# Kernel optimization log

Measured on AMD Instinct MI355X. Metric: run time of the kernel, lower is better.

Reference implementation:

```python
import jax, jax.numpy as jnp
import numpy as np

B, S, C = 16, 2048, 256      # batch, seq_len, in_channels
QK, H = 256, 8               # qk_dim, num_heads
N, ED = 512, 256             # envbook_num+1, envbook_dim
D = QK // H                  # per_head_dim
SCALING = QK ** (-0.5)       # note: original scales by full qk_dim, not per-head dim


def setup_inputs() -> dict:
    key = jax.random.key(0)
    k1, k2, k3, k4 = jax.random.split(key, 4)
    x = jax.random.normal(k1, (B, S, C), dtype=jnp.float32)
    env_codebook = jax.random.normal(k2, (N, ED), dtype=jnp.float32)
    # nn.Linear weights stored transposed for x @ W convention
    Wq = jax.random.normal(k3, (C, QK), dtype=jnp.float32) * (1.0 / np.sqrt(C))
    Wk = jax.random.normal(k4, (ED, QK), dtype=jnp.float32) * (1.0 / np.sqrt(ED))
    return {"x": x, "env_codebook": env_codebook, "Wq": Wq, "Wk": Wk}


def reference(x, env_codebook, Wq, Wk):
    # query: [B,S,QK] -> [B,S,H,D]; key: [N,QK] -> [N,H,D]
    q = (x @ Wq).reshape(B, S, H, D)
    k = (env_codebook @ Wk).reshape(N, H, D)
    # scores: [B,H,S,N]
    scores = jnp.einsum("bshd,nhd->bhsn", q, k) * SCALING
    probs = jax.nn.softmax(scores, axis=-1)
    causal_att = probs[..., 0]          # [B,H,S]
    env_selects = probs[..., 1:]        # [B,H,S,N-1]
    env_att = env_selects.sum(axis=-1)  # [B,H,S]
    return (env_att, causal_att, env_selects)
```

## Files before the change

### kernel.cpp

```cpp
#include <hip/hip_runtime.h>
#include <hip/hip_bf16.h>

#define B_  16
#define S_  2048
#define C_  256
#define QK_ 256
#define H_  8
#define N_  512
#define D_  32

typedef short  bf16x8 __attribute__((ext_vector_type(8)));
typedef float  f32x4  __attribute__((ext_vector_type(4)));

__device__ __forceinline__ unsigned short f2bf(float f) {
    union { float f; unsigned u; } v; v.f = f;
    unsigned r = v.u + 0x7fffu + ((v.u >> 16) & 1u);
    return (unsigned short)(r >> 16);
}

__global__ void k_convert_x(const float* __restrict__ x,
                            unsigned short* __restrict__ xbf) {
    int i = blockIdx.x * blockDim.x + threadIdx.x;
    float4 v = ((const float4*)x)[i];
    ushort4 o;
    o.x = f2bf(v.x); o.y = f2bf(v.y); o.z = f2bf(v.z); o.w = f2bf(v.w);
    ((ushort4*)xbf)[i] = o;
}

__global__ void k_wqt(const float* __restrict__ Wq,
                      unsigned short* __restrict__ wqt) {
    int n = blockIdx.x, c = threadIdx.x;
    wqt[n * 256 + c] = f2bf(Wq[c * 256 + n]);
}

__global__ void k_kproj(const float* __restrict__ env,
                        const float* __restrict__ Wk,
                        unsigned short* __restrict__ kbf) {
    __shared__ float erow[256];
    int n = blockIdx.x, t = threadIdx.x;
    erow[t] = env[n * 256 + t];
    __syncthreads();
    float acc = 0.f;
#pragma unroll 8
    for (int c = 0; c < 256; ++c) acc += erow[c] * Wk[c * 256 + t];
    int h = t >> 5, d = t & 31;
    kbf[(h * N_ + n) * D_ + d] = f2bf(acc);
}

__global__ __launch_bounds__(256) void k_qproj(
        const unsigned short* __restrict__ xbf,
        const unsigned short* __restrict__ wqt,
        unsigned short* __restrict__ qws) {
    int tid  = threadIdx.x;
    int lane = tid & 63, w = tid >> 6;
    int l15  = lane & 15, quad = lane >> 4;
    int r0   = blockIdx.x * 16;
    int nb   = w * 64;

    const unsigned short* arow = xbf + (size_t)(r0 + l15) * 256 + quad * 8;
    const unsigned short* brow[4];
#pragma unroll
    for (int nt = 0; nt < 4; ++nt)
        brow[nt] = wqt + (size_t)(nb + nt * 16 + l15) * 256 + quad * 8;

    f32x4 acc[4] = {};
#pragma unroll
    for (int kk = 0; kk < 8; ++kk) {
        bf16x8 a = *(const bf16x8*)(arow + kk * 32);
#pragma unroll
        for (int nt = 0; nt < 4; ++nt) {
            bf16x8 b = *(const bf16x8*)(brow[nt] + kk * 32);
            acc[nt] = __builtin_amdgcn_mfma_f32_16x16x32_bf16(a, b, acc[nt], 0, 0, 0);
        }
    }
#pragma unroll
    for (int nt = 0; nt < 4; ++nt) {
        int col = nb + nt * 16 + l15;
        int h = col >> 5, d = col & 31;
#pragma unroll
        for (int r = 0; r < 4; ++r) {
            int gr = r0 + quad * 4 + r;
            int b = gr >> 11, s = gr & 2047;
            qws[(((size_t)(b * H_ + h)) * S_ + s) * D_ + d] = f2bf(acc[nt][r] * 0.0625f);
        }
    }
}

__global__ __launch_bounds__(256) void k_scores(
        const unsigned short* __restrict__ qws,
        const unsigned short* __restrict__ kbf,
        float* __restrict__ out) {
    float* env_att = out;
    float* causal  = out + (size_t)B_ * H_ * S_;
    float* es      = out + (size_t)2 * B_ * H_ * S_;

    int tid  = threadIdx.x;
    int lane = tid & 63, w = tid >> 6;
    int l15  = lane & 15, quad = lane >> 4;

    int bid  = blockIdx.x;
    int bh   = bid >> 4;
    int sblk = (bid & 15) * 128;
    int h    = bh & 7;

    __shared__ float red[4][16];

    const unsigned short* kb = kbf + (size_t)h * N_ * D_;
    int nb = w * 128;
    bf16x8 bf[8];
#pragma unroll
    for (int j = 0; j < 8; ++j)
        bf[j] = *(const bf16x8*)(kb + (size_t)(nb + j * 16 + l15) * D_ + quad * 8);

    const unsigned short* qbase = qws + (size_t)bh * S_ * D_;

    for (int st = 0; st < 8; ++st) {
        int s0 = sblk + st * 16;
        bf16x8 a = *(const bf16x8*)(qbase + (size_t)(s0 + l15) * D_ + quad * 8);

        f32x4 c[8];
#pragma unroll
        for (int j = 0; j < 8; ++j) {
            f32x4 z = {};
            c[j] = __builtin_amdgcn_mfma_f32_16x16x32_bf16(a, bf[j], z, 0, 0, 0);
        }
        float psum[4] = {0.f, 0.f, 0.f, 0.f};
#pragma unroll
        for (int j = 0; j < 8; ++j)
#pragma unroll
            for (int r = 0; r < 4; ++r) {
                float e = __expf(c[j][r]);
                c[j][r] = e;
                psum[r] += e;
            }
#pragma unroll
        for (int off = 1; off < 16; off <<= 1)
#pragma unroll
            for (int r = 0; r < 4; ++r)
                psum[r] += __shfl_xor(psum[r], off, 64);
        if (l15 == 0) {
#pragma unroll
            for (int r = 0; r < 4; ++r) red[w][quad * 4 + r] = psum[r];
        }
        __syncthreads();
        float inv[4];
#pragma unroll
        for (int r = 0; r < 4; ++r) {
            int row = quad * 4 + r;
            float tot = red[0][row] + red[1][row] + red[2][row] + red[3][row];
            inv[r] = 1.0f / tot;
        }
        __syncthreads();

        int srow = bh * S_ + s0 + quad * 4;
#pragma unroll
        for (int j = 0; j < 8; ++j) {
            int n = nb + j * 16 + l15;
#pragma unroll
            for (int r = 0; r < 4; ++r) {
                float p = c[j][r] * inv[r];
                if (n > 0) es[(size_t)(srow + r) * 511 + (n - 1)] = p;
            }
        }
        if (w == 0 && l15 == 0) {
#pragma unroll
            for (int r = 0; r < 4; ++r) {
                float p0 = c[0][r] * inv[r];
                causal[srow + r]  = p0;
                env_att[srow + r] = 1.0f - p0;
            }
        }
    }
}

extern "C" void kernel_launch(void* const* d_in, const int* in_sizes, int n_in,
                              void* d_out, int out_size, void* d_ws, size_t ws_size,
                              hipStream_t stream) {
    const float* x   = (const float*)d_in[0];
    const float* env = (const float*)d_in[1];
    const float* Wq  = (const float*)d_in[2];
    const float* Wk  = (const float*)d_in[3];
    float* out = (float*)d_out;

    char* ws = (char*)d_ws;
    unsigned short* xbf = (unsigned short*)(ws);
    unsigned short* qws = (unsigned short*)(ws + 16777216);
    unsigned short* kbf = (unsigned short*)(ws + 33554432);
    unsigned short* wqt = (unsigned short*)(ws + 33816576);

    k_convert_x<<<8192, 256, 0, stream>>>(x, xbf);
    k_wqt      <<<256,  256, 0, stream>>>(Wq, wqt);
    k_kproj    <<<512,  256, 0, stream>>>(env, Wk, kbf);
    k_qproj    <<<2048, 256, 0, stream>>>(xbf, wqt, qws);
    k_scores   <<<2048, 256, 0, stream>>>(qws, kbf, out);
}
```

Measured before the change: 669.9 us.

## Fuse x conversion into Q projection, merge prep kernels, stage score stores in LDS

```diff
diff --git a/kernel.cpp b/kernel.cpp
--- a/kernel.cpp
+++ b/kernel.cpp
@@ -18,37 +18,29 @@
     return (unsigned short)(r >> 16);
 }
 
-__global__ void k_convert_x(const float* __restrict__ x,
-                            unsigned short* __restrict__ xbf) {
-    int i = blockIdx.x * blockDim.x + threadIdx.x;
-    float4 v = ((const float4*)x)[i];
-    ushort4 o;
-    o.x = f2bf(v.x); o.y = f2bf(v.y); o.z = f2bf(v.z); o.w = f2bf(v.w);
-    ((ushort4*)xbf)[i] = o;
-}
-
-__global__ void k_wqt(const float* __restrict__ Wq,
-                      unsigned short* __restrict__ wqt) {
-    int n = blockIdx.x, c = threadIdx.x;
-    wqt[n * 256 + c] = f2bf(Wq[c * 256 + n]);
-}
-
-__global__ void k_kproj(const float* __restrict__ env,
-                        const float* __restrict__ Wk,
-                        unsigned short* __restrict__ kbf) {
+__global__ void k_prep(const float* __restrict__ Wq,
+                       const float* __restrict__ env,
+                       const float* __restrict__ Wk,
+                       unsigned short* __restrict__ wqt,
+                       unsigned short* __restrict__ kbf) {
     __shared__ float erow[256];
-    int n = blockIdx.x, t = threadIdx.x;
-    erow[t] = env[n * 256 + t];
-    __syncthreads();
-    float acc = 0.f;
+    int bid = blockIdx.x, t = threadIdx.x;
+    if (bid < 256) {
+        wqt[bid * 256 + t] = f2bf(Wq[t * 256 + bid]);
+    } else {
+        int n = bid - 256;
+        erow[t] = env[n * 256 + t];
+        __syncthreads();
+        float acc = 0.f;
 #pragma unroll 8
-    for (int c = 0; c < 256; ++c) acc += erow[c] * Wk[c * 256 + t];
-    int h = t >> 5, d = t & 31;
-    kbf[(h * N_ + n) * D_ + d] = f2bf(acc);
+        for (int c = 0; c < 256; ++c) acc += erow[c] * Wk[c * 256 + t];
+        int h = t >> 5, d = t & 31;
+        kbf[(h * N_ + n) * D_ + d] = f2bf(acc);
+    }
 }
 
 __global__ __launch_bounds__(256) void k_qproj(
-        const unsigned short* __restrict__ xbf,
+        const float* __restrict__ x,
         const unsigned short* __restrict__ wqt,
         unsigned short* __restrict__ qws) {
     int tid  = threadIdx.x;
@@ -57,7 +49,7 @@
     int r0   = blockIdx.x * 16;
     int nb   = w * 64;
 
-    const unsigned short* arow = xbf + (size_t)(r0 + l15) * 256 + quad * 8;
+    const float* arow = x + (size_t)(r0 + l15) * 256 + quad * 8;
     const unsigned short* brow[4];
 #pragma unroll
     for (int nt = 0; nt < 4; ++nt)
@@ -66,7 +58,13 @@
     f32x4 acc[4] = {};
 #pragma unroll
     for (int kk = 0; kk < 8; ++kk) {
-        bf16x8 a = *(const bf16x8*)(arow + kk * 32);
+        float4 f0 = *(const float4*)(arow + kk * 32);
+        float4 f1 = *(const float4*)(arow + kk * 32 + 4);
+        bf16x8 a;
+        a[0] = (short)f2bf(f0.x); a[1] = (short)f2bf(f0.y);
+        a[2] = (short)f2bf(f0.z); a[3] = (short)f2bf(f0.w);
+        a[4] = (short)f2bf(f1.x); a[5] = (short)f2bf(f1.y);
+        a[6] = (short)f2bf(f1.z); a[7] = (short)f2bf(f1.w);
 #pragma unroll
         for (int nt = 0; nt < 4; ++nt) {
             bf16x8 b = *(const bf16x8*)(brow[nt] + kk * 32);
@@ -86,6 +84,7 @@
     }
 }
 
+#define PADW 514
 __global__ __launch_bounds__(256) void k_scores(
         const unsigned short* __restrict__ qws,
         const unsigned short* __restrict__ kbf,
@@ -93,6 +92,9 @@
     float* env_att = out;
     float* causal  = out + (size_t)B_ * H_ * S_;
     float* es      = out + (size_t)2 * B_ * H_ * S_;
+
+    __shared__ float red[4][16];
+    __shared__ float tile[16 * PADW];
 
     int tid  = threadIdx.x;
     int lane = tid & 63, w = tid >> 6;
@@ -102,8 +104,6 @@
     int bh   = bid >> 4;
     int sblk = (bid & 15) * 128;
     int h    = bh & 7;
-
-    __shared__ float red[4][16];
 
     const unsigned short* kb = kbf + (size_t)h * N_ * D_;
     int nb = w * 128;
@@ -150,25 +150,29 @@
             float tot = red[0][row] + red[1][row] + red[2][row] + red[3][row];
             inv[r] = 1.0f / tot;
         }
-        __syncthreads();
-
-        int srow = bh * S_ + s0 + quad * 4;
 #pragma unroll
         for (int j = 0; j < 8; ++j) {
             int n = nb + j * 16 + l15;
 #pragma unroll
-            for (int r = 0; r < 4; ++r) {
-                float p = c[j][r] * inv[r];
-                if (n > 0) es[(size_t)(srow + r) * 511 + (n - 1)] = p;
-            }
+            for (int r = 0; r < 4; ++r)
+                tile[(quad * 4 + r) * PADW + n] = c[j][r] * inv[r];
         }
         if (w == 0 && l15 == 0) {
+            int srow = bh * S_ + s0 + quad * 4;
 #pragma unroll
             for (int r = 0; r < 4; ++r) {
                 float p0 = c[0][r] * inv[r];
                 causal[srow + r]  = p0;
                 env_att[srow + r] = 1.0f - p0;
             }
+        }
+        __syncthreads();
+        size_t region = ((size_t)bh * S_ + s0) * 511;
+#pragma unroll
+        for (int row = 0; row < 16; ++row) {
+            es[region + row * 511 + tid] = tile[row * PADW + 1 + tid];
+            if (tid < 255)
+                es[region + row * 511 + 256 + tid] = tile[row * PADW + 257 + tid];
         }
     }
 }
@@ -183,14 +187,11 @@
     float* out = (float*)d_out;
 
     char* ws = (char*)d_ws;
-    unsigned short* xbf = (unsigned short*)(ws);
-    unsigned short* qws = (unsigned short*)(ws + 16777216);
-    unsigned short* kbf = (unsigned short*)(ws + 33554432);
-    unsigned short* wqt = (unsigned short*)(ws + 33816576);
+    unsigned short* qws = (unsigned short*)(ws);
+    unsigned short* kbf = (unsigned short*)(ws + 16777216);
+    unsigned short* wqt = (unsigned short*)(ws + 17039360);
 
-    k_convert_x<<<8192, 256, 0, stream>>>(x, xbf);
-    k_wqt      <<<256,  256, 0, stream>>>(Wq, wqt);
-    k_kproj    <<<512,  256, 0, stream>>>(env, Wk, kbf);
-    k_qproj    <<<2048, 256, 0, stream>>>(xbf, wqt, qws);
-    k_scores   <<<2048, 256, 0, stream>>>(qws, kbf, out);
+    k_prep  <<<768,  256, 0, stream>>>(Wq, env, Wk, wqt, kbf);
+    k_qproj <<<2048, 256, 0, stream>>>(x, wqt, qws);
+    k_scores<<<2048, 256, 0, stream>>>(qws, kbf, out);
 }
```

Result: faster. 635.5 us (-5.1%).
